# Kernel tuning notes

Measured on AMD Instinct MI355X. Metric: run time of the kernel, lower is better.

The kernel has to match this reference:

```python
import jax, jax.numpy as jnp
import numpy as np

B, N, C, H = 32, 577, 768, 12
D = C // H  # head_dim = 64


def _rotate_half(t):
    half = t.shape[-1] // 2
    return jnp.concatenate([-t[..., half:], t[..., :half]], axis=-1)


def _rope(t, sin, cos):
    # t: [B, H, N-1, D]; sin/cos: [N-1, D] broadcast over batch and heads
    return t * cos + _rotate_half(t) * sin


def setup_inputs() -> dict:
    key = jax.random.key(0)
    ks = jax.random.split(key, 5)
    x = jax.random.normal(ks[0], (B, N, C), dtype=jnp.float32)
    w_qkv = jax.random.normal(ks[1], (C, 3 * C), dtype=jnp.float32) * (1.0 / np.sqrt(C))
    b_qkv = jnp.zeros((3 * C,), dtype=jnp.float32)
    w_proj = jax.random.normal(ks[2], (C, C), dtype=jnp.float32) * (1.0 / np.sqrt(C))
    b_proj = jnp.zeros((C,), dtype=jnp.float32)
    # rotary tables for the N-1 non-CLS tokens
    pos = jnp.arange(N - 1, dtype=jnp.float32)[:, None]            # [N-1, 1]
    inv_freq = 1.0 / (10000.0 ** (jnp.arange(0, D, 2, dtype=jnp.float32) / D))  # [D/2]
    ang = pos * inv_freq[None, :]                                   # [N-1, D/2]
    ang = jnp.concatenate([ang, ang], axis=-1)                      # [N-1, D]
    rope_sin = jnp.sin(ang)
    rope_cos = jnp.cos(ang)
    return {"x": x, "w_qkv": w_qkv, "b_qkv": b_qkv, "w_proj": w_proj,
            "b_proj": b_proj, "rope_sin": rope_sin, "rope_cos": rope_cos}


def reference(x, w_qkv, b_qkv, w_proj, b_proj, rope_sin, rope_cos):
    Bx, Nx, Cx = x.shape
    qkv = x @ w_qkv + b_qkv                                   # [B, N, 3C]
    qkv = qkv.reshape(Bx, Nx, 3, H, D).transpose(2, 0, 3, 1, 4)  # [3, B, H, N, D]
    q, k, v = qkv[0], qkv[1], qkv[2]
    # RoPE only on non-CLS tokens (index 0 is CLS)
    q = jnp.concatenate([q[:, :, :1, :], _rope(q[:, :, 1:, :], rope_sin, rope_cos)], axis=2)
    k = jnp.concatenate([k[:, :, :1, :], _rope(k[:, :, 1:, :], rope_sin, rope_cos)], axis=2)
    q = q / jnp.sqrt(jnp.float32(D))
    attn = jnp.einsum("bhqd,bhkd->bhqk", q, k)               # [B, H, N, N]
    attn = jax.nn.softmax(attn.astype(jnp.float32), axis=-1).astype(x.dtype)
    out = jnp.einsum("bhqk,bhkd->bhqd", attn, v)             # [B, H, N, D]
    out = out.transpose(0, 2, 1, 3).reshape(Bx, Nx, Cx)       # [B, N, C]
    return out @ w_proj + b_proj
```

## Files before the change

### kernel.cpp

```cpp
#include <hip/hip_runtime.h>

#define Bdim 32
#define Ndim 577
#define Cdim 768
#define Hdim 12
#define Ddim 64
#define Mdim (Bdim*Ndim)
#define VSTRIDE 640
#define TSTRIDE 152
#define QSCALE 0.18033688f
#define MGRP 19

typedef __attribute__((ext_vector_type(4))) float f32x4;
typedef __attribute__((ext_vector_type(8))) __bf16 bf16x8;
typedef __attribute__((ext_vector_type(4))) __bf16 bf16x4;

__device__ __forceinline__ void gl_lds16(const __bf16* g, __bf16* l) {
  __builtin_amdgcn_global_load_lds((const __attribute__((address_space(1))) void*)g,
                                   (__attribute__((address_space(3))) void*)l, 16, 0, 0);
}

__global__ __launch_bounds__(256) void f32_to_bf16(const float4* __restrict__ in,
                                                   bf16x4* __restrict__ out, int n4) {
  int i = blockIdx.x * 256 + threadIdx.x;
  if (i < n4) {
    float4 v = in[i];
    bf16x4 o = {(__bf16)v.x, (__bf16)v.y, (__bf16)v.z, (__bf16)v.w};
    out[i] = o;
  }
}

__global__ __launch_bounds__(256) void transpose_f32_bf16(const float* __restrict__ in,
                                                          __bf16* __restrict__ out,
                                                          int R, int Cc) {
  __shared__ float tile[64][65];
  int bx = blockIdx.x * 64;
  int by = blockIdx.y * 64;
  int tx = threadIdx.x & 63, ty = threadIdx.x >> 6;
  for (int i = ty; i < 64; i += 4) {
    int r = by + i, c = bx + tx;
    tile[i][tx] = (r < R && c < Cc) ? in[(size_t)r * Cc + c] : 0.f;
  }
  __syncthreads();
  for (int i = ty; i < 64; i += 4) {
    int r = bx + i, c = by + tx;
    if (r < Cc && c < R) out[(size_t)r * R + c] = (__bf16)tile[tx][i];
  }
}

__device__ __forceinline__ void gemm_bt_core(const __bf16* __restrict__ A,
                                             const __bf16* __restrict__ BT,
                                             int m0, int n0,
                                             __bf16* As, __bf16* Bs,
                                             f32x4 acc[4][4]) {
  const int t = threadIdx.x;
  const int lane = t & 63, w = t >> 6;
  const int quad = lane >> 4, l16 = lane & 15;
  const int wm = w >> 1, wn = w & 1;

  for (int k0 = 0; k0 < 768; k0 += 64) {
    __syncthreads();
    #pragma unroll
    for (int e = 0; e < 4; ++e) {
      int h = e >> 1;
      int j = ((e & 1) << 2) | w;
      int row = j * 16 + (lane >> 2);
      int col = k0 + h * 32 + (lane & 3) * 8;
      int ar = m0 + row; if (ar > Mdim - 1) ar = Mdim - 1;
      __bf16* dstA = As + h * 4096 + j * 512 + lane * 8;
      __bf16* dstB = Bs + h * 4096 + j * 512 + lane * 8;
      gl_lds16(A  + (size_t)ar * 768 + col, dstA);
      gl_lds16(BT + (size_t)(n0 + row) * 768 + col, dstB);
    }
    __syncthreads();
    #pragma unroll
    for (int s = 0; s < 2; ++s) {
      bf16x8 a[4], b[4];
      #pragma unroll
      for (int i = 0; i < 4; ++i) {
        a[i] = *(const bf16x8*)(As + s * 4096 + (wm * 64 + i * 16 + l16) * 32 + quad * 8);
        b[i] = *(const bf16x8*)(Bs + s * 4096 + (wn * 64 + i * 16 + l16) * 32 + quad * 8);
      }
      #pragma unroll
      for (int mt = 0; mt < 4; ++mt)
        #pragma unroll
        for (int nt = 0; nt < 4; ++nt)
          acc[mt][nt] = __builtin_amdgcn_mfma_f32_16x16x32_bf16(a[mt], b[nt], acc[mt][nt], 0, 0, 0);
    }
  }
}

__device__ __forceinline__ bool xcd_decode(int lin, int nb, int mb, int& n, int& m) {
  int x8 = lin & 7;
  int rest = lin >> 3;
  n = rest % nb;
  int mg = rest / nb;
  m = mg * 8 + x8;
  return m < mb;
}

__global__ __launch_bounds__(256) void qk_kernel(const __bf16* __restrict__ x,
                                                 const __bf16* __restrict__ wqkvT,
                                                 const float* __restrict__ b_qkv,
                                                 const float* __restrict__ rs,
                                                 const float* __restrict__ rc,
                                                 __bf16* __restrict__ q,
                                                 __bf16* __restrict__ k) {
  __shared__ __bf16 As[2 * 128 * 32];
  __shared__ __bf16 Bs[2 * 128 * 32];
  int nb, mbk;
  if (!xcd_decode(blockIdx.x, 12, 145, nb, mbk)) return;
  const int n0 = nb * 128, m0 = mbk * 128;

  f32x4 acc[4][4];
  const f32x4 fz = {0.f, 0.f, 0.f, 0.f};
  for (int i = 0; i < 4; ++i) for (int j = 0; j < 4; ++j) acc[i][j] = fz;
  gemm_bt_core(x, wqkvT, m0, n0, As, Bs, acc);

  const int lane = threadIdx.x & 63, w = threadIdx.x >> 6;
  const int quad = lane >> 4, l16 = lane & 15;
  const int wm = w >> 1, wn = w & 1;
  const int colbase = n0 + wn * 64;
  const int matrix = colbase / 768;
  const int head = (colbase % 768) / 64;

  #pragma unroll
  for (int mt = 0; mt < 4; ++mt) {
    int mbase = m0 + wm * 64 + mt * 16 + quad * 4;
    #pragma unroll
    for (int r = 0; r < 4; ++r) {
      int m = mbase + r;
      if (m >= Mdim) continue;
      int bb = m / 577, tok = m % 577;
      #pragma unroll
      for (int nt = 0; nt < 4; ++nt) {
        int d = nt * 16 + l16;
        float val = acc[mt][nt][r] + b_qkv[colbase + d];
        if (tok > 0) {
          float partner = acc[mt][nt ^ 2][r] + b_qkv[colbase + (d ^ 32)];
          float sn = rs[(size_t)(tok - 1) * 64 + d];
          float cs = rc[(size_t)(tok - 1) * 64 + d];
          float rot = (d < 32) ? -partner : partner;
          val = val * cs + rot * sn;
        }
        __bf16* dst;
        if (matrix == 0) { val *= QSCALE; dst = q; } else dst = k;
        dst[((size_t)(bb * 12 + head) * 577 + tok) * 64 + d] = (__bf16)val;
      }
    }
  }
}

__global__ __launch_bounds__(256) void v_kernel(const __bf16* __restrict__ x,
                                                const __bf16* __restrict__ wqkvT,
                                                const float* __restrict__ b_qkv,
                                                __bf16* __restrict__ vt) {
  __shared__ __bf16 As[2 * 128 * 32];
  __shared__ __bf16 Bs[2 * 128 * 32];
  __shared__ __bf16 Ts[64 * TSTRIDE];
  int nb, mbk;
  if (!xcd_decode(blockIdx.x, 6, 145, nb, mbk)) return;
  const int n0 = 1536 + nb * 128, m0 = mbk * 128;

  f32x4 acc[4][4];
  const f32x4 fz = {0.f, 0.f, 0.f, 0.f};
  for (int i = 0; i < 4; ++i) for (int j = 0; j < 4; ++j) acc[i][j] = fz;
  gemm_bt_core(x, wqkvT, m0, n0, As, Bs, acc);

  const int t = threadIdx.x;
  const int lane = t & 63, w = t >> 6;
  const int quad = lane >> 4, l16 = lane & 15;
  const int wm = w >> 1, wn = w & 1;
  const int colbase = n0 + wn * 64;

  #pragma unroll
  for (int h = 0; h < 2; ++h) {
    __syncthreads();
    if (wn == h) {
      #pragma unroll
      for (int mt = 0; mt < 4; ++mt) {
        int tokbase = wm * 64 + mt * 16 + quad * 4;
        #pragma unroll
        for (int r = 0; r < 4; ++r) {
          #pragma unroll
          for (int nt = 0; nt < 4; ++nt) {
            int dl = nt * 16 + l16;
            Ts[dl * TSTRIDE + tokbase + r] =
                (__bf16)(acc[mt][nt][r] + b_qkv[colbase + dl]);
          }
        }
      }
    }
    __syncthreads();
    int hh = (n0 + h * 64 - 1536) / 64;
    #pragma unroll
    for (int it = 0; it < 4; ++it) {
      int c = it * 256 + t;
      int dl = c >> 4, chunk = c & 15;
      bf16x8 vv = *(const bf16x8*)(Ts + dl * TSTRIDE + chunk * 8);
      #pragma unroll
      for (int j = 0; j < 8; ++j) {
        int m = m0 + chunk * 8 + j;
        if (m < Mdim) {
          int bb = m / 577, tok = m % 577;
          vt[((size_t)(bb * 12 + hh) * 64 + dl) * VSTRIDE + tok] = vv[j];
        }
      }
    }
  }
}

__global__ __launch_bounds__(256) void attn_kernel(const __bf16* __restrict__ q,
                                                   const __bf16* __restrict__ k,
                                                   const __bf16* __restrict__ vt,
                                                   __bf16* __restrict__ ao) {
  __shared__ __bf16 qs[4096];
  __shared__ __bf16 ks[4096];
  __shared__ __bf16 vs[4096];
  __shared__ __bf16 ps[64 * 72];

  const int x8 = blockIdx.x & 7;
  const int rest = blockIdx.x >> 3;
  const int qt = rest % 10;
  const int bh = (rest / 10) * 8 + x8;

  const int t = threadIdx.x;
  const int lane = t & 63, w = t >> 6;
  const int quad = lane >> 4, l16 = lane & 15;

  const __bf16* qbase = q + (size_t)bh * 577 * 64;
  const __bf16* kbase = k + (size_t)bh * 577 * 64;
  const __bf16* vbase = vt + (size_t)bh * 64 * VSTRIDE;

  #pragma unroll
  for (int p = 0; p < 2; ++p) {
    int g = p * 256 + t;
    int d8 = g >> 6, tok = g & 63;
    gl_lds16(qbase + (size_t)(qt * 64 + tok) * 64 + d8 * 8, qs + (size_t)g * 8);
  }

  f32x4 O[4]; const f32x4 fz = {0.f, 0.f, 0.f, 0.f};
  for (int i = 0; i < 4; ++i) O[i] = fz;
  float l_part[4] = {0.f, 0.f, 0.f, 0.f};

  for (int kt = 0; kt < 10; ++kt) {
    __syncthreads();
    #pragma unroll
    for (int p = 0; p < 2; ++p) {
      int g = p * 256 + t;
      int d8 = g >> 6, tok = g & 63;
      gl_lds16(kbase + (size_t)(kt * 64 + tok) * 64 + d8 * 8, ks + (size_t)g * 8);
      gl_lds16(vbase + (size_t)(g & 63) * VSTRIDE + kt * 64 + (g >> 6) * 8, vs + (size_t)g * 8);
    }
    __syncthreads();

    f32x4 S[4]; for (int i = 0; i < 4; ++i) S[i] = fz;
    #pragma unroll
    for (int step = 0; step < 2; ++step) {
      bf16x8 a = *(const bf16x8*)(qs + (size_t)((step * 4 + quad) * 64 + w * 16 + l16) * 8);
      #pragma unroll
      for (int nt = 0; nt < 4; ++nt) {
        bf16x8 b = *(const bf16x8*)(ks + (size_t)((step * 4 + quad) * 64 + nt * 16 + l16) * 8);
        S[nt] = __builtin_amdgcn_mfma_f32_16x16x32_bf16(a, b, S[nt], 0, 0, 0);
      }
    }

    int kv_left = 577 - kt * 64;
    if (kv_left < 64) {
      #pragma unroll
      for (int nt = 0; nt < 4; ++nt) {
        int c = nt * 16 + l16;
        if (c >= kv_left) { S[nt][0] = -1e30f; S[nt][1] = -1e30f; S[nt][2] = -1e30f; S[nt][3] = -1e30f; }
      }
    }

    #pragma unroll
    for (int r = 0; r < 4; ++r) {
      #pragma unroll
      for (int nt = 0; nt < 4; ++nt) {
        float e = exp2f(S[nt][r]);
        l_part[r] += e;
        ps[(size_t)(w * 16 + quad * 4 + r) * 72 + nt * 16 + l16] = (__bf16)e;
      }
    }

    #pragma unroll
    for (int step = 0; step < 2; ++step) {
      bf16x8 a = *(const bf16x8*)(ps + (size_t)(w * 16 + l16) * 72 + step * 32 + quad * 8);
      #pragma unroll
      for (int dt = 0; dt < 4; ++dt) {
        bf16x8 b = *(const bf16x8*)(vs + (size_t)((step * 4 + quad) * 64 + dt * 16 + l16) * 8);
        O[dt] = __builtin_amdgcn_mfma_f32_16x16x32_bf16(a, b, O[dt], 0, 0, 0);
      }
    }
  }

  const int bb = bh / 12, hh = bh % 12;
  const int qrow0 = qt * 64 + w * 16 + quad * 4;
  #pragma unroll
  for (int r = 0; r < 4; ++r) {
    float l = l_part[r];
    l += __shfl_xor(l, 1); l += __shfl_xor(l, 2);
    l += __shfl_xor(l, 4); l += __shfl_xor(l, 8);
    int row = qrow0 + r;
    if (row < 577) {
      float inv = 1.f / l;
      size_t base = ((size_t)(bb * 577 + row)) * 768 + hh * 64;
      #pragma unroll
      for (int dt = 0; dt < 4; ++dt)
        ao[base + dt * 16 + l16] = (__bf16)(O[dt][r] * inv);
    }
  }
}

__global__ __launch_bounds__(256) void proj_kernel(const __bf16* __restrict__ ao,
                                                   const __bf16* __restrict__ wprojT,
                                                   const float* __restrict__ b_proj,
                                                   float* __restrict__ out) {
  __shared__ __bf16 As[2 * 128 * 32];
  __shared__ __bf16 Bs[2 * 128 * 32];
  int nb, mbk;
  if (!xcd_decode(blockIdx.x, 6, 145, nb, mbk)) return;
  const int n0 = nb * 128, m0 = mbk * 128;

  f32x4 acc[4][4];
  const f32x4 fz = {0.f, 0.f, 0.f, 0.f};
  for (int i = 0; i < 4; ++i) for (int j = 0; j < 4; ++j) acc[i][j] = fz;
  gemm_bt_core(ao, wprojT, m0, n0, As, Bs, acc);

  const int lane = threadIdx.x & 63, w = threadIdx.x >> 6;
  const int quad = lane >> 4, l16 = lane & 15;
  const int wm = w >> 1, wn = w & 1;
  const int colbase = n0 + wn * 64;

  #pragma unroll
  for (int mt = 0; mt < 4; ++mt) {
    int mbase = m0 + wm * 64 + mt * 16 + quad * 4;
    #pragma unroll
    for (int r = 0; r < 4; ++r) {
      int m = mbase + r;
      if (m >= Mdim) continue;
      #pragma unroll
      for (int nt = 0; nt < 4; ++nt) {
        int c = colbase + nt * 16 + l16;
        out[(size_t)m * 768 + c] = acc[mt][nt][r] + b_proj[c];
      }
    }
  }
}

extern "C" void kernel_launch(void* const* d_in, const int* in_sizes, int n_in,
                              void* d_out, int out_size, void* d_ws, size_t ws_size,
                              hipStream_t stream) {
  const float* x      = (const float*)d_in[0];
  const float* w_qkv  = (const float*)d_in[1];
  const float* b_qkv  = (const float*)d_in[2];
  const float* w_proj = (const float*)d_in[3];
  const float* b_proj = (const float*)d_in[4];
  const float* rsn    = (const float*)d_in[5];
  const float* rcs    = (const float*)d_in[6];
  float* out = (float*)d_out;

  constexpr size_t QK_E = (size_t)Bdim * Hdim * Ndim * Ddim;
  constexpr size_t VT_E = (size_t)Bdim * Hdim * Ddim * VSTRIDE;
  constexpr size_t AO_E = (size_t)Mdim * Cdim;
  __bf16* q      = (__bf16*)d_ws;
  __bf16* k      = q + QK_E;
  __bf16* vt     = k + QK_E;
  __bf16* ao     = vt + VT_E;
  __bf16* xb     = ao;
  __bf16* wqkvT  = ao + AO_E;
  __bf16* wprojT = wqkvT + (size_t)2304 * 768;

  f32_to_bf16<<<13848, 256, 0, stream>>>((const float4*)x, (bf16x4*)xb,
                                         (int)(AO_E / 4));
  transpose_f32_bf16<<<dim3(36, 12), 256, 0, stream>>>(w_qkv, wqkvT, 768, 2304);
  transpose_f32_bf16<<<dim3(12, 12), 256, 0, stream>>>(w_proj, wprojT, 768, 768);
  qk_kernel<<<8 * MGRP * 12, 256, 0, stream>>>(xb, wqkvT, b_qkv, rsn, rcs, q, k);
  v_kernel<<<8 * MGRP * 6, 256, 0, stream>>>(xb, wqkvT, b_qkv, vt);
  attn_kernel<<<3840, 256, 0, stream>>>(q, k, vt, ao);
  proj_kernel<<<8 * MGRP * 6, 256, 0, stream>>>(ao, wprojT, b_proj, out);
}
```

Measured before the change: 445.9 us.

## Double-buffer GEMM LDS tiles and XOR-swizzle K chunks to avoid bank conflicts

The shared GEMM core now prefetches the next K tile into a second LDS buffer while MFMAs run on the current one, which cuts one barrier per iteration and overlaps global-to-LDS loads with compute. It also XOR-swizzles the 8-element K-chunk placement on both the store and read side to reduce LDS bank conflicts. LDS per block doubles to 64KB, which can lower occupancy. The V kernel reuses the A buffer for its transpose staging instead of a separate array.

```diff
diff --git a/kernel.cpp b/kernel.cpp
--- a/kernel.cpp
+++ b/kernel.cpp
@@ -48,6 +48,25 @@
   }
 }
 
+__device__ __forceinline__ void stage_tile(const __bf16* __restrict__ A,
+                                           const __bf16* __restrict__ BT,
+                                           int m0, int n0, int k0,
+                                           __bf16* As, __bf16* Bs) {
+  const int t = threadIdx.x;
+  const int lane = t & 63, w = t >> 6;
+  const int cs = (lane & 3) ^ ((lane >> 2) & 3) ^ ((lane >> 4) & 3);
+  #pragma unroll
+  for (int e = 0; e < 4; ++e) {
+    int h = e >> 1;
+    int j = ((e & 1) << 2) | w;
+    int row = j * 16 + (lane >> 2);
+    int col = k0 + h * 32 + cs * 8;
+    int ar = m0 + row; if (ar > Mdim - 1) ar = Mdim - 1;
+    gl_lds16(A  + (size_t)ar * 768 + col, As + h * 4096 + j * 512 + lane * 8);
+    gl_lds16(BT + (size_t)(n0 + row) * 768 + col, Bs + h * 4096 + j * 512 + lane * 8);
+  }
+}
+
 __device__ __forceinline__ void gemm_bt_core(const __bf16* __restrict__ A,
                                              const __bf16* __restrict__ BT,
                                              int m0, int n0,
@@ -57,29 +76,21 @@
   const int lane = t & 63, w = t >> 6;
   const int quad = lane >> 4, l16 = lane & 15;
   const int wm = w >> 1, wn = w & 1;
-
+  const int ksw = (quad ^ (l16 & 3) ^ ((l16 >> 2) & 3)) << 3;
+
+  stage_tile(A, BT, m0, n0, 0, As, Bs);
+  __syncthreads();
   for (int k0 = 0; k0 < 768; k0 += 64) {
-    __syncthreads();
-    #pragma unroll
-    for (int e = 0; e < 4; ++e) {
-      int h = e >> 1;
-      int j = ((e & 1) << 2) | w;
-      int row = j * 16 + (lane >> 2);
-      int col = k0 + h * 32 + (lane & 3) * 8;
-      int ar = m0 + row; if (ar > Mdim - 1) ar = Mdim - 1;
-      __bf16* dstA = As + h * 4096 + j * 512 + lane * 8;
-      __bf16* dstB = Bs + h * 4096 + j * 512 + lane * 8;
-      gl_lds16(A  + (size_t)ar * 768 + col, dstA);
-      gl_lds16(BT + (size_t)(n0 + row) * 768 + col, dstB);
-    }
-    __syncthreads();
+    const int buf = (k0 >> 6) & 1;
+    if (k0 < 704)
+      stage_tile(A, BT, m0, n0, k0 + 64, As + (buf ^ 1) * 8192, Bs + (buf ^ 1) * 8192);
     #pragma unroll
     for (int s = 0; s < 2; ++s) {
       bf16x8 a[4], b[4];
       #pragma unroll
       for (int i = 0; i < 4; ++i) {
-        a[i] = *(const bf16x8*)(As + s * 4096 + (wm * 64 + i * 16 + l16) * 32 + quad * 8);
-        b[i] = *(const bf16x8*)(Bs + s * 4096 + (wn * 64 + i * 16 + l16) * 32 + quad * 8);
+        a[i] = *(const bf16x8*)(As + buf * 8192 + s * 4096 + (wm * 64 + i * 16 + l16) * 32 + ksw);
+        b[i] = *(const bf16x8*)(Bs + buf * 8192 + s * 4096 + (wn * 64 + i * 16 + l16) * 32 + ksw);
       }
       #pragma unroll
       for (int mt = 0; mt < 4; ++mt)
@@ -87,6 +98,7 @@
         for (int nt = 0; nt < 4; ++nt)
           acc[mt][nt] = __builtin_amdgcn_mfma_f32_16x16x32_bf16(a[mt], b[nt], acc[mt][nt], 0, 0, 0);
     }
+    __syncthreads();
   }
 }
 
@@ -106,8 +118,8 @@
                                                  const float* __restrict__ rc,
                                                  __bf16* __restrict__ q,
                                                  __bf16* __restrict__ k) {
-  __shared__ __bf16 As[2 * 128 * 32];
-  __shared__ __bf16 Bs[2 * 128 * 32];
+  __shared__ __bf16 As[2 * 2 * 128 * 32];
+  __shared__ __bf16 Bs[2 * 2 * 128 * 32];
   int nb, mbk;
   if (!xcd_decode(blockIdx.x, 12, 145, nb, mbk)) return;
   const int n0 = nb * 128, m0 = mbk * 128;
@@ -155,9 +167,9 @@
                                                 const __bf16* __restrict__ wqkvT,
                                                 const float* __restrict__ b_qkv,
                                                 __bf16* __restrict__ vt) {
-  __shared__ __bf16 As[2 * 128 * 32];
-  __shared__ __bf16 Bs[2 * 128 * 32];
-  __shared__ __bf16 Ts[64 * TSTRIDE];
+  __shared__ __bf16 As[2 * 2 * 128 * 32];
+  __shared__ __bf16 Bs[2 * 2 * 128 * 32];
+  __bf16* Ts = As;
   int nb, mbk;
   if (!xcd_decode(blockIdx.x, 6, 145, nb, mbk)) return;
   const int n0 = 1536 + nb * 128, m0 = mbk * 128;
@@ -317,8 +329,8 @@
                                                    const __bf16* __restrict__ wprojT,
                                                    const float* __restrict__ b_proj,
                                                    float* __restrict__ out) {
-  __shared__ __bf16 As[2 * 128 * 32];
-  __shared__ __bf16 Bs[2 * 128 * 32];
+  __shared__ __bf16 As[2 * 2 * 128 * 32];
+  __shared__ __bf16 Bs[2 * 2 * 128 * 32];
   int nb, mbk;
   if (!xcd_decode(blockIdx.x, 6, 145, nb, mbk)) return;
   const int n0 = nb * 128, m0 = mbk * 128;
```

Measured after the change: 474.8 us. 1.06x slower.

## Rewrite projection GEMMs as 256x256 tiles with pipelined swizzled LDS staging

Applied to the files above, without the earlier changes.

Replaces the 128x128 four-wave GEMM core with a 256x256 eight-wave core that double-buffers half-tiles in XOR-swizzled LDS. Loads for the next k-steps are interleaved with MFMA phases, controlled by explicit waitcnt, barriers and setprio. The QK weight columns are permuted during the transpose so each rotary partner sits in the same wave's adjacent fragment, and the V epilogue transposes through swizzled LDS. The aim is more data reuse per tile and overlap of global loads with compute. In exchange it uses 128KB of LDS per block and far fewer blocks (73x6, 73x3), which risks wave quantization across CUs and a tail of padded rows.

```diff
diff --git a/kernel.cpp b/kernel.cpp
--- a/kernel.cpp
+++ b/kernel.cpp
@@ -7,9 +7,8 @@
 #define Ddim 64
 #define Mdim (Bdim*Ndim)
 #define VSTRIDE 640
-#define TSTRIDE 152
 #define QSCALE 0.18033688f
-#define MGRP 19
+#define NT 12
 
 typedef __attribute__((ext_vector_type(4))) float f32x4;
 typedef __attribute__((ext_vector_type(8))) __bf16 bf16x8;
@@ -32,14 +31,19 @@
 
 __global__ __launch_bounds__(256) void transpose_f32_bf16(const float* __restrict__ in,
                                                           __bf16* __restrict__ out,
-                                                          int R, int Cc) {
+                                                          int R, int Cc, int permqk) {
   __shared__ float tile[64][65];
   int bx = blockIdx.x * 64;
   int by = blockIdx.y * 64;
   int tx = threadIdx.x & 63, ty = threadIdx.x >> 6;
   for (int i = ty; i < 64; i += 4) {
     int r = by + i, c = bx + tx;
-    tile[i][tx] = (r < R && c < Cc) ? in[(size_t)r * Cc + c] : 0.f;
+    int cl = c;
+    if (permqk && c < 1536) {
+      int p = c & 63;
+      cl = (c & ~63) | ((p & 15) | ((p & 16) << 1) | ((p & 32) >> 1));
+    }
+    tile[i][tx] = (r < R && c < Cc) ? in[(size_t)r * Cc + cl] : 0.f;
   }
   __syncthreads();
   for (int i = ty; i < 64; i += 4) {
@@ -48,163 +52,230 @@
   }
 }
 
-__device__ __forceinline__ void gemm_bt_core(const __bf16* __restrict__ A,
+
+#define HSLOT(b,h) (((b)*2+(h))*8192)
+
+__device__ __forceinline__ void stageA(const __bf16* __restrict__ A, int m0,
+                                       int k0, int h, __bf16* lds, int tid) {
+  #pragma unroll
+  for (int i = 0; i < 2; ++i) {
+    int idx = i * 512 + tid;
+    int rl = idx >> 3, c = idx & 7;
+    int row = m0 + h * 128 + rl;
+    if (row > Mdim - 1) row = Mdim - 1;
+    gl_lds16(A + (size_t)row * 768 + k0 + ((c ^ (rl & 7)) << 3), lds + (idx << 3));
+  }
+}
+
+__device__ __forceinline__ void stageB(const __bf16* __restrict__ BT, int n0,
+                                       int k0, int h, __bf16* lds, int tid) {
+  #pragma unroll
+  for (int i = 0; i < 2; ++i) {
+    int idx = i * 512 + tid;
+    int rl = idx >> 3, c = idx & 7;
+    int row = n0 + h * 128 + rl;
+    gl_lds16(BT + (size_t)row * 768 + k0 + ((c ^ (rl & 7)) << 3), lds + (idx << 3));
+  }
+}
+
+__device__ __forceinline__ void gemm256_core(const __bf16* __restrict__ A,
                                              const __bf16* __restrict__ BT,
                                              int m0, int n0,
-                                             __bf16* As, __bf16* Bs,
-                                             f32x4 acc[4][4]) {
-  const int t = threadIdx.x;
-  const int lane = t & 63, w = t >> 6;
+                                             __bf16* __restrict__ smA,
+                                             __bf16* __restrict__ smB,
+                                             f32x4 (&acc)[2][4][2][2]) {
+  const int tid = threadIdx.x;
+  const int lane = tid & 63, w = tid >> 6;
   const int quad = lane >> 4, l16 = lane & 15;
-  const int wm = w >> 1, wn = w & 1;
-
-  for (int k0 = 0; k0 < 768; k0 += 64) {
-    __syncthreads();
-    #pragma unroll
-    for (int e = 0; e < 4; ++e) {
-      int h = e >> 1;
-      int j = ((e & 1) << 2) | w;
-      int row = j * 16 + (lane >> 2);
-      int col = k0 + h * 32 + (lane & 3) * 8;
-      int ar = m0 + row; if (ar > Mdim - 1) ar = Mdim - 1;
-      __bf16* dstA = As + h * 4096 + j * 512 + lane * 8;
-      __bf16* dstB = Bs + h * 4096 + j * 512 + lane * 8;
-      gl_lds16(A  + (size_t)ar * 768 + col, dstA);
-      gl_lds16(BT + (size_t)(n0 + row) * 768 + col, dstB);
-    }
-    __syncthreads();
-    #pragma unroll
-    for (int s = 0; s < 2; ++s) {
-      bf16x8 a[4], b[4];
-      #pragma unroll
-      for (int i = 0; i < 4; ++i) {
-        a[i] = *(const bf16x8*)(As + s * 4096 + (wm * 64 + i * 16 + l16) * 32 + quad * 8);
-        b[i] = *(const bf16x8*)(Bs + s * 4096 + (wn * 64 + i * 16 + l16) * 32 + quad * 8);
-      }
-      #pragma unroll
-      for (int mt = 0; mt < 4; ++mt)
-        #pragma unroll
-        for (int nt = 0; nt < 4; ++nt)
-          acc[mt][nt] = __builtin_amdgcn_mfma_f32_16x16x32_bf16(a[mt], b[nt], acc[mt][nt], 0, 0, 0);
-    }
-  }
-}
-
-__device__ __forceinline__ bool xcd_decode(int lin, int nb, int mb, int& n, int& m) {
-  int x8 = lin & 7;
-  int rest = lin >> 3;
-  n = rest % nb;
-  int mg = rest / nb;
-  m = mg * 8 + x8;
-  return m < mb;
-}
-
-__global__ __launch_bounds__(256) void qk_kernel(const __bf16* __restrict__ x,
-                                                 const __bf16* __restrict__ wqkvT,
-                                                 const float* __restrict__ b_qkv,
-                                                 const float* __restrict__ rs,
-                                                 const float* __restrict__ rc,
-                                                 __bf16* __restrict__ q,
-                                                 __bf16* __restrict__ k) {
-  __shared__ __bf16 As[2 * 128 * 32];
-  __shared__ __bf16 Bs[2 * 128 * 32];
-  int nb, mbk;
-  if (!xcd_decode(blockIdx.x, 12, 145, nb, mbk)) return;
-  const int n0 = nb * 128, m0 = mbk * 128;
-
-  f32x4 acc[4][4];
+  const int wm = w >> 2, wn = w & 3;
+
+  stageA(A, m0, 0, 0, smA + HSLOT(0, 0), tid);
+  stageA(A, m0, 0, 1, smA + HSLOT(0, 1), tid);
+  stageB(BT, n0, 0, 0, smB + HSLOT(0, 0), tid);
+  stageB(BT, n0, 0, 1, smB + HSLOT(0, 1), tid);
+  stageA(A, m0, 64, 0, smA + HSLOT(1, 0), tid);
+  stageB(BT, n0, 64, 1, smB + HSLOT(1, 1), tid);
+  asm volatile("s_waitcnt vmcnt(4)" ::: "memory");
+  __builtin_amdgcn_s_barrier();
+
+  const int arow = wm * 64 + l16;
+  const int brow = wn * 32 + l16;
+  const int kx = ((quad ^ (l16 & 7)) << 3);
+
+  #pragma unroll 2
+  for (int t = 0; t < NT; ++t) {
+    const int buf = t & 1;
+    #pragma unroll
+    for (int ph = 0; ph < 4; ++ph) {
+      const int qi = ph >> 1;
+      const int qj = (ph == 1 || ph == 2) ? 1 : 0;
+      const __bf16* Ab = smA + HSLOT(buf, qi);
+      const __bf16* Bb = smB + HSLOT(buf, qj);
+      bf16x8 a[4][2], b[2][2];
+      #pragma unroll
+      for (int mf = 0; mf < 4; ++mf) {
+        a[mf][0] = *(const bf16x8*)(Ab + (arow + mf * 16) * 64 + kx);
+        a[mf][1] = *(const bf16x8*)(Ab + (arow + mf * 16) * 64 + (kx ^ 32));
+      }
+      #pragma unroll
+      for (int nf = 0; nf < 2; ++nf) {
+        b[nf][0] = *(const bf16x8*)(Bb + (brow + nf * 16) * 64 + kx);
+        b[nf][1] = *(const bf16x8*)(Bb + (brow + nf * 16) * 64 + (kx ^ 32));
+      }
+      if (ph == 0) { if (t + 1 < NT) stageA(A, m0, (t + 1) << 6, 1, smA + HSLOT((t + 1) & 1, 1), tid); }
+      if (ph == 1) { if (t + 1 < NT) stageB(BT, n0, (t + 1) << 6, 0, smB + HSLOT((t + 1) & 1, 0), tid); }
+      if (ph == 2) { if (t + 2 < NT) stageA(A, m0, (t + 2) << 6, 0, smA + HSLOT(buf, 0), tid); }
+      if (ph == 3) {
+        if (t + 2 < NT) stageB(BT, n0, (t + 2) << 6, 1, smB + HSLOT(buf, 1), tid);
+        if (t < NT - 2)       { asm volatile("s_waitcnt vmcnt(4)" ::: "memory"); }
+        else if (t == NT - 2) { asm volatile("s_waitcnt vmcnt(0)" ::: "memory"); }
+        __builtin_amdgcn_sched_barrier(0);
+      }
+      __builtin_amdgcn_s_barrier();
+      asm volatile("s_waitcnt lgkmcnt(0)" ::: "memory");
+      __builtin_amdgcn_sched_barrier(0);
+      __builtin_amdgcn_s_setprio(1);
+      #pragma unroll
+      for (int ks = 0; ks < 2; ++ks)
+        #pragma unroll
+        for (int mf = 0; mf < 4; ++mf)
+          #pragma unroll
+          for (int nf = 0; nf < 2; ++nf)
+            acc[qi][mf][qj][nf] = __builtin_amdgcn_mfma_f32_16x16x32_bf16(
+                a[mf][ks], b[nf][ks], acc[qi][mf][qj][nf], 0, 0, 0);
+      __builtin_amdgcn_s_setprio(0);
+      __builtin_amdgcn_s_barrier();
+    }
+  }
+}
+
+
+__global__ __launch_bounds__(512, 2) void qk_kernel(const __bf16* __restrict__ x,
+                                                    const __bf16* __restrict__ wqkvT,
+                                                    const float* __restrict__ b_qkv,
+                                                    const float* __restrict__ rs,
+                                                    const float* __restrict__ rc,
+                                                    __bf16* __restrict__ q,
+                                                    __bf16* __restrict__ k) {
+  __shared__ __bf16 sm[65536];
+  const int nb = blockIdx.x % 6, mb = blockIdx.x / 6;
+  const int n0 = nb * 256, m0 = mb * 256;
+
+  f32x4 acc[2][4][2][2];
   const f32x4 fz = {0.f, 0.f, 0.f, 0.f};
-  for (int i = 0; i < 4; ++i) for (int j = 0; j < 4; ++j) acc[i][j] = fz;
-  gemm_bt_core(x, wqkvT, m0, n0, As, Bs, acc);
+  #pragma unroll
+  for (int i = 0; i < 2; ++i)
+    #pragma unroll
+    for (int j = 0; j < 4; ++j)
+      #pragma unroll
+      for (int u = 0; u < 2; ++u)
+        #pragma unroll
+        for (int v = 0; v < 2; ++v) acc[i][j][u][v] = fz;
+
+  gemm256_core(x, wqkvT, m0, n0, sm, sm + 32768, acc);
 
   const int lane = threadIdx.x & 63, w = threadIdx.x >> 6;
   const int quad = lane >> 4, l16 = lane & 15;
-  const int wm = w >> 1, wn = w & 1;
-  const int colbase = n0 + wn * 64;
-  const int matrix = colbase / 768;
-  const int head = (colbase % 768) / 64;
-
-  #pragma unroll
-  for (int mt = 0; mt < 4; ++mt) {
-    int mbase = m0 + wm * 64 + mt * 16 + quad * 4;
-    #pragma unroll
-    for (int r = 0; r < 4; ++r) {
-      int m = mbase + r;
-      if (m >= Mdim) continue;
-      int bb = m / 577, tok = m % 577;
-      #pragma unroll
-      for (int nt = 0; nt < 4; ++nt) {
-        int d = nt * 16 + l16;
-        float val = acc[mt][nt][r] + b_qkv[colbase + d];
-        if (tok > 0) {
-          float partner = acc[mt][nt ^ 2][r] + b_qkv[colbase + (d ^ 32)];
-          float sn = rs[(size_t)(tok - 1) * 64 + d];
-          float cs = rc[(size_t)(tok - 1) * 64 + d];
-          float rot = (d < 32) ? -partner : partner;
-          val = val * cs + rot * sn;
-        }
-        __bf16* dst;
-        if (matrix == 0) { val *= QSCALE; dst = q; } else dst = k;
-        dst[((size_t)(bb * 12 + head) * 577 + tok) * 64 + d] = (__bf16)val;
-      }
-    }
-  }
-}
-
-__global__ __launch_bounds__(256) void v_kernel(const __bf16* __restrict__ x,
-                                                const __bf16* __restrict__ wqkvT,
-                                                const float* __restrict__ b_qkv,
-                                                __bf16* __restrict__ vt) {
-  __shared__ __bf16 As[2 * 128 * 32];
-  __shared__ __bf16 Bs[2 * 128 * 32];
-  __shared__ __bf16 Ts[64 * TSTRIDE];
-  int nb, mbk;
-  if (!xcd_decode(blockIdx.x, 6, 145, nb, mbk)) return;
-  const int n0 = 1536 + nb * 128, m0 = mbk * 128;
-
-  f32x4 acc[4][4];
-  const f32x4 fz = {0.f, 0.f, 0.f, 0.f};
-  for (int i = 0; i < 4; ++i) for (int j = 0; j < 4; ++j) acc[i][j] = fz;
-  gemm_bt_core(x, wqkvT, m0, n0, As, Bs, acc);
-
-  const int t = threadIdx.x;
-  const int lane = t & 63, w = t >> 6;
-  const int quad = lane >> 4, l16 = lane & 15;
-  const int wm = w >> 1, wn = w & 1;
-  const int colbase = n0 + wn * 64;
-
-  #pragma unroll
-  for (int h = 0; h < 2; ++h) {
-    __syncthreads();
-    if (wn == h) {
-      #pragma unroll
-      for (int mt = 0; mt < 4; ++mt) {
-        int tokbase = wm * 64 + mt * 16 + quad * 4;
-        #pragma unroll
-        for (int r = 0; r < 4; ++r) {
+  const int wm = w >> 2, wn = w & 3;
+
+  #pragma unroll
+  for (int qi = 0; qi < 2; ++qi)
+    #pragma unroll
+    for (int mf = 0; mf < 4; ++mf) {
+      int mbase = m0 + qi * 128 + wm * 64 + mf * 16 + quad * 4;
+      #pragma unroll
+      for (int qj = 0; qj < 2; ++qj)
+        #pragma unroll
+        for (int nf = 0; nf < 2; ++nf) {
+          int col = n0 + qj * 128 + wn * 32 + nf * 16 + l16;
+          int matrix = col / 768;
+          int within = col % 768;
+          int head = within / 64, p = within % 64;
+          int d = (p & 15) | ((p & 16) << 1) | ((p & 32) >> 1);
+          float bias   = b_qkv[matrix * 768 + head * 64 + d];
+          float bias_p = b_qkv[matrix * 768 + head * 64 + (d ^ 32)];
           #pragma unroll
-          for (int nt = 0; nt < 4; ++nt) {
-            int dl = nt * 16 + l16;
-            Ts[dl * TSTRIDE + tokbase + r] =
-                (__bf16)(acc[mt][nt][r] + b_qkv[colbase + dl]);
+          for (int r = 0; r < 4; ++r) {
+            int m = mbase + r;
+            if (m >= Mdim) continue;
+            int bb = m / 577, tok = m % 577;
+            float val = acc[qi][mf][qj][nf][r] + bias;
+            if (tok > 0) {
+              float partner = acc[qi][mf][qj][nf ^ 1][r] + bias_p;
+              float sn = rs[(size_t)(tok - 1) * 64 + d];
+              float cs = rc[(size_t)(tok - 1) * 64 + d];
+              float rot = (p & 16) ? partner : -partner;
+              val = val * cs + rot * sn;
+            }
+            __bf16* dst;
+            if (matrix == 0) { val *= QSCALE; dst = q; } else dst = k;
+            dst[((size_t)(bb * 12 + head) * 577 + tok) * 64 + d] = (__bf16)val;
           }
         }
-      }
-    }
-    __syncthreads();
-    int hh = (n0 + h * 64 - 1536) / 64;
-    #pragma unroll
-    for (int it = 0; it < 4; ++it) {
-      int c = it * 256 + t;
-      int dl = c >> 4, chunk = c & 15;
-      bf16x8 vv = *(const bf16x8*)(Ts + dl * TSTRIDE + chunk * 8);
-      #pragma unroll
-      for (int j = 0; j < 8; ++j) {
-        int m = m0 + chunk * 8 + j;
-        if (m < Mdim) {
-          int bb = m / 577, tok = m % 577;
-          vt[((size_t)(bb * 12 + hh) * 64 + dl) * VSTRIDE + tok] = vv[j];
+    }
+}
+
+__global__ __launch_bounds__(512, 2) void v_kernel(const __bf16* __restrict__ x,
+                                                   const __bf16* __restrict__ wqkvT,
+                                                   const float* __restrict__ b_qkv,
+                                                   __bf16* __restrict__ vt) {
+  __shared__ __bf16 sm[65536];
+  const int nb = blockIdx.x % 3, mb = blockIdx.x / 3;
+  const int n0loc = nb * 256;
+  const int n0abs = 1536 + n0loc;
+  const int m0 = mb * 256;
+
+  f32x4 acc[2][4][2][2];
+  const f32x4 fz = {0.f, 0.f, 0.f, 0.f};
+  #pragma unroll
+  for (int i = 0; i < 2; ++i)
+    #pragma unroll
+    for (int j = 0; j < 4; ++j)
+      #pragma unroll
+      for (int u = 0; u < 2; ++u)
+        #pragma unroll
+        for (int v = 0; v < 2; ++v) acc[i][j][u][v] = fz;
+
+  gemm256_core(x, wqkvT, m0, n0abs, sm, sm + 32768, acc);
+
+  const int tid = threadIdx.x;
+  const int lane = tid & 63, w = tid >> 6;
+  const int quad = lane >> 4, l16 = lane & 15;
+  const int wm = w >> 2, wn = w & 3;
+  char* smc = (char*)sm;
+
+  #pragma unroll
+  for (int qi = 0; qi < 2; ++qi)
+    #pragma unroll
+    for (int mf = 0; mf < 4; ++mf) {
+      int tk = qi * 128 + wm * 64 + mf * 16 + quad * 4;
+      #pragma unroll
+      for (int qj = 0; qj < 2; ++qj)
+        #pragma unroll
+        for (int nf = 0; nf < 2; ++nf) {
+          int cl = qj * 128 + wn * 32 + nf * 16 + l16;
+          float bias = b_qkv[1536 + n0loc + cl];
+          f32x4 av = acc[qi][mf][qj][nf];
+          bf16x4 pk = {(__bf16)(av[0] + bias), (__bf16)(av[1] + bias),
+                       (__bf16)(av[2] + bias), (__bf16)(av[3] + bias)};
+          *(bf16x4*)(smc + ((cl * 512 + tk * 2) ^ ((cl & 7) << 4))) = pk;
         }
+    }
+  __syncthreads();
+
+  #pragma unroll
+  for (int it = 0; it < 16; ++it) {
+    int g = it * 512 + tid;
+    int cl = g >> 5, ch = g & 31;
+    bf16x8 vv = *(const bf16x8*)(smc + ((cl * 512 + ch * 16) ^ ((cl & 7) << 4)));
+    int col = n0loc + cl;
+    int head = col >> 6, dl = col & 63;
+    #pragma unroll
+    for (int j = 0; j < 8; ++j) {
+      int m = m0 + ch * 8 + j;
+      if (m < Mdim) {
+        int bb = m / 577, tok = m % 577;
+        vt[((size_t)(bb * 12 + head) * 64 + dl) * VSTRIDE + tok] = vv[j];
       }
     }
   }
@@ -313,40 +384,49 @@
   }
 }
 
-__global__ __launch_bounds__(256) void proj_kernel(const __bf16* __restrict__ ao,
-                                                   const __bf16* __restrict__ wprojT,
-                                                   const float* __restrict__ b_proj,
-                                                   float* __restrict__ out) {
-  __shared__ __bf16 As[2 * 128 * 32];
-  __shared__ __bf16 Bs[2 * 128 * 32];
-  int nb, mbk;
-  if (!xcd_decode(blockIdx.x, 6, 145, nb, mbk)) return;
-  const int n0 = nb * 128, m0 = mbk * 128;
-
-  f32x4 acc[4][4];
+__global__ __launch_bounds__(512, 2) void proj_kernel(const __bf16* __restrict__ ao,
+                                                      const __bf16* __restrict__ wprojT,
+                                                      const float* __restrict__ b_proj,
+                                                      float* __restrict__ out) {
+  __shared__ __bf16 sm[65536];
+  const int nb = blockIdx.x % 3, mb = blockIdx.x / 3;
+  const int n0 = nb * 256, m0 = mb * 256;
+
+  f32x4 acc[2][4][2][2];
   const f32x4 fz = {0.f, 0.f, 0.f, 0.f};
-  for (int i = 0; i < 4; ++i) for (int j = 0; j < 4; ++j) acc[i][j] = fz;
-  gemm_bt_core(ao, wprojT, m0, n0, As, Bs, acc);
+  #pragma unroll
+  for (int i = 0; i < 2; ++i)
+    #pragma unroll
+    for (int j = 0; j < 4; ++j)
+      #pragma unroll
+      for (int u = 0; u < 2; ++u)
+        #pragma unroll
+        for (int v = 0; v < 2; ++v) acc[i][j][u][v] = fz;
+
+  gemm256_core(ao, wprojT, m0, n0, sm, sm + 32768, acc);
 
   const int lane = threadIdx.x & 63, w = threadIdx.x >> 6;
   const int quad = lane >> 4, l16 = lane & 15;
-  const int wm = w >> 1, wn = w & 1;
-  const int colbase = n0 + wn * 64;
-
-  #pragma unroll
-  for (int mt = 0; mt < 4; ++mt) {
-    int mbase = m0 + wm * 64 + mt * 16 + quad * 4;
-    #pragma unroll
-    for (int r = 0; r < 4; ++r) {
-      int m = mbase + r;
-      if (m >= Mdim) continue;
-      #pragma unroll
-      for (int nt = 0; nt < 4; ++nt) {
-        int c = colbase + nt * 16 + l16;
-        out[(size_t)m * 768 + c] = acc[mt][nt][r] + b_proj[c];
-      }
-    }
-  }
+  const int wm = w >> 2, wn = w & 3;
+
+  #pragma unroll
+  for (int qi = 0; qi < 2; ++qi)
+    #pragma unroll
+    for (int mf = 0; mf < 4; ++mf) {
+      int mbase = m0 + qi * 128 + wm * 64 + mf * 16 + quad * 4;
+      #pragma unroll
+      for (int qj = 0; qj < 2; ++qj)
+        #pragma unroll
+        for (int nf = 0; nf < 2; ++nf) {
+          int col = n0 + qj * 128 + wn * 32 + nf * 16 + l16;
+          float bias = b_proj[col];
+          #pragma unroll
+          for (int r = 0; r < 4; ++r) {
+            int m = mbase + r;
+            if (m < Mdim) out[(size_t)m * 768 + col] = acc[qi][mf][qj][nf][r] + bias;
+          }
+        }
+    }
 }
 
 extern "C" void kernel_launch(void* const* d_in, const int* in_sizes, int n_in,
@@ -374,10 +454,10 @@
 
   f32_to_bf16<<<13848, 256, 0, stream>>>((const float4*)x, (bf16x4*)xb,
                                          (int)(AO_E / 4));
-  transpose_f32_bf16<<<dim3(36, 12), 256, 0, stream>>>(w_qkv, wqkvT, 768, 2304);
-  transpose_f32_bf16<<<dim3(12, 12), 256, 0, stream>>>(w_proj, wprojT, 768, 768);
-  qk_kernel<<<8 * MGRP * 12, 256, 0, stream>>>(xb, wqkvT, b_qkv, rsn, rcs, q, k);
-  v_kernel<<<8 * MGRP * 6, 256, 0, stream>>>(xb, wqkvT, b_qkv, vt);
+  transpose_f32_bf16<<<dim3(36, 12), 256, 0, stream>>>(w_qkv, wqkvT, 768, 2304, 1);
+  transpose_f32_bf16<<<dim3(12, 12), 256, 0, stream>>>(w_proj, wprojT, 768, 768, 0);
+  qk_kernel<<<73 * 6, 512, 0, stream>>>(xb, wqkvT, b_qkv, rsn, rcs, q, k);
+  v_kernel<<<73 * 3, 512, 0, stream>>>(xb, wqkvT, b_qkv, vt);
   attn_kernel<<<3840, 256, 0, stream>>>(q, k, vt, ao);
-  proj_kernel<<<8 * MGRP * 6, 256, 0, stream>>>(ao, wprojT, b_proj, out);
-}
+  proj_kernel<<<73 * 3, 512, 0, stream>>>(ao, wprojT, b_proj, out);
+}
```

Measured after the change: 462.0 us. 1.04x slower.
